# Kernel tuning notes

Measured on AMD Instinct MI355X. Metric: run time of the kernel, lower is better.

Reference implementation:

```python
import jax, jax.numpy as jnp
import numpy as np

EPS = 1e-15


def _trace(t):
    return jnp.einsum('bii->b', t)


def _ortho_loss(ss, k):
    n = jnp.linalg.norm(ss, axis=(-1, -2), keepdims=True)
    diff = ss / n - jnp.eye(k, dtype=ss.dtype) / np.float32(np.sqrt(k))
    return jnp.mean(jnp.linalg.norm(diff, axis=(-1, -2)))


def _mincut_terms(s, adj):
    out_adj = jnp.einsum('bnk,bnm,bml->bkl', s, adj, s)
    d_flat = adj.sum(-1)  # degrees [B,N]
    num = _trace(out_adj)
    den = _trace(jnp.einsum('bnk,bn,bnl->bkl', s, d_flat, s)) + EPS
    return out_adj, num, den, d_flat


def dense_mincut_rewiring(x, adj, s, mask):
    k = s.shape[-1]  # 2
    m = mask[..., None].astype(x.dtype)
    s = jax.nn.softmax(s, axis=-1) * m
    _, num, den, _ = _mincut_terms(s, adj)
    mincut_loss = -jnp.mean(num / den)
    ortho_loss = _ortho_loss(jnp.einsum('bnk,bnl->bkl', s, s), k)
    # laplacian derivative of spectral gap wrt A_uv: (f_u - f_v)^2, f = soft bipartition
    f = s[..., 0]
    dlam = (f[:, :, None] - f[:, None, :]) ** 2
    return adj * (1.0 - dlam), mincut_loss, ortho_loss


def dense_CT_rewiring(x, adj, s, mask):
    k = s.shape[-1]
    m = mask[..., None].astype(x.dtype)
    s = jax.nn.softmax(s, axis=-1) * m
    d_flat = adj.sum(-1)
    sds = _trace(jnp.einsum('bnk,bn,bnl->bkl', s, d_flat, s))
    sas = _trace(jnp.einsum('bnk,bnm,bml->bkl', s, adj, s))
    den = _trace(jnp.einsum('bnk,bnl->bkl', s, s)) + EPS
    ct_loss = jnp.mean((sds - sas) / den)  # tr(Z^T L Z) / tr(Z^T Z)
    ortho_loss = _ortho_loss(jnp.einsum('bnk,bnl->bkl', s, s), k)
    # pairwise CT distances ||z_u - z_v|| / vol(G), sparsified by A
    sq = (s * s).sum(-1)
    d2 = sq[:, :, None] + sq[:, None, :] - 2.0 * jnp.einsum('bnk,bmk->bnm', s, s)
    ct_dist = jnp.sqrt(jnp.maximum(d2, 0.0) + 1e-12)
    vol = d_flat.sum(-1)
    new_adj = (ct_dist / (vol[:, None, None] + EPS)) * adj
    return new_adj, ct_loss, ortho_loss


def dense_mincut_pool(x, adj, s, mask):
    k = s.shape[-1]
    m = mask[..., None].astype(x.dtype)
    s = jax.nn.softmax(s, axis=-1) * m
    x = x * m
    out = jnp.einsum('bnk,bnf->bkf', s, x)
    out_adj, num, den, _ = _mincut_terms(s, adj)
    mincut_loss = -jnp.mean(num / den)
    ortho_loss = _ortho_loss(jnp.einsum('bnk,bnl->bkl', s, s), k)
    out_adj = out_adj * (1.0 - jnp.eye(k, dtype=adj.dtype))  # zero diagonal
    d = jnp.sqrt(out_adj.sum(-1)) + EPS  # [B,k]
    out_adj = out_adj / d[:, None, :] / d[:, :, None]
    return out, out_adj, mincut_loss, ortho_loss


def _dgc(x, adj, w_rel, b_rel, w_root):
    # DenseGraphConv(aggr='add'): lin_rel(A @ x) + lin_root(x)
    return jnp.matmul(adj, x) @ w_rel + b_rel + x @ w_root


def setup_inputs() -> dict:
    B, N, IN, H, KC, OUT, KMC = 16, 1024, 128, 32, 32, 10, 16
    keys = iter(jax.random.split(jax.random.key(0), 48))

    def lin(fin, fout):
        lim = float(1.0 / np.sqrt(fin))
        return (jax.random.uniform(next(keys), (fin, fout), jnp.float32, -lim, lim),
                jax.random.uniform(next(keys), (fout,), jnp.float32, -lim, lim))

    x = jax.random.normal(next(keys), (B, N, IN), jnp.float32)
    u = jax.random.uniform(next(keys), (B, N, N), jnp.float32)
    a = (u < 0.0156).astype(jnp.float32)  # avg degree ~16
    adj = jnp.maximum(a, jnp.swapaxes(a, 1, 2)) * (1.0 - jnp.eye(N, dtype=jnp.float32))
    mask = jnp.ones((B, N), dtype=bool)
    W1, b1 = lin(IN, H)
    Wrw, brw = lin(H, 2)
    Wg_rel, bg = lin(H, H); Wg_root, _ = lin(H, H)
    Wmcg, bmcg = lin(H, KMC)
    W2g_rel, b2g = lin(H, H); W2g_root, _ = lin(H, H)
    Wct, bct = lin(H, KC)
    Wc_rel, bc = lin(H, H); Wc_root, _ = lin(H, H)
    Wmcc, bmcc = lin(H, KMC)
    Wcat, bcat = lin(2 * H, H)
    W2, b2 = lin(H, H)
    W3, b3 = lin(H, OUT)
    return dict(x=x, adj=adj, mask=mask, W1=W1, b1=b1, Wrw=Wrw, brw=brw,
                Wg_rel=Wg_rel, bg=bg, Wg_root=Wg_root, Wmcg=Wmcg, bmcg=bmcg,
                W2g_rel=W2g_rel, b2g=b2g, W2g_root=W2g_root, Wct=Wct, bct=bct,
                Wc_rel=Wc_rel, bc=bc, Wc_root=Wc_root, Wmcc=Wmcc, bmcc=bmcc,
                Wcat=Wcat, bcat=bcat, W2=W2, b2=b2, W3=W3, b3=b3)


def reference(x, adj, mask, W1, b1, Wrw, brw, Wg_rel, bg, Wg_root, Wmcg, bmcg,
              W2g_rel, b2g, W2g_root, Wct, bct, Wc_rel, bc, Wc_root, Wmcc, bmcc,
              Wcat, bcat, W2, b2, W3, b3):
    x = x @ W1 + b1
    # GAP branch
    adj_gap, mc_rw, ol_rw = dense_mincut_rewiring(x, adj, x @ Wrw + brw, mask)
    x_gap = _dgc(x, adj_gap, Wg_rel, bg, Wg_root)
    x_gap, adj_gap, mc1, ol1 = dense_mincut_pool(x_gap, adj_gap, x_gap @ Wmcg + bmcg, mask)
    x_gap = _dgc(x_gap, adj_gap, W2g_rel, b2g, W2g_root)
    # CT branch
    adj_ct, ct_loss, ol_ct = dense_CT_rewiring(x, adj, x @ Wct + bct, mask)
    x_ct = _dgc(x, adj_ct, Wc_rel, bc, Wc_root)
    x_ct, adj_ct, mc2, ol2 = dense_mincut_pool(x_ct, adj_ct, x_ct @ Wmcc + bmcc, mask)
    x_ct = _dgc(x_ct, adj_ct, W2g_rel, b2g, W2g_root)  # source reuses self.conv2gap here
    h = jax.nn.relu(jnp.concatenate([x_gap, x_ct], axis=2) @ Wcat + bcat).sum(axis=1)
    h = jax.nn.relu(h @ W2 + b2)
    logits = h @ W3 + b3
    main_loss = mc_rw + ct_loss + mc1 + mc2
    ortho_loss = ol_rw + ol_ct + ol1 + ol2
    return (jax.nn.log_softmax(logits, axis=-1), main_loss, ortho_loss)
```

## Files before the change

### kernel.cpp

```cpp
#include <hip/hip_runtime.h>
#include <math.h>

#define BB   16
#define NNODE 1024
#define INF_ 128
#define HH   32
#define KMC  16
#define CAP  128
#define EPS15 1e-15f

typedef float v4f __attribute__((ext_vector_type(4)));

#define OFF_X      0
#define OFF_SRW    524288
#define OFF_SQCT   557056
#define OFF_SCT    573440
#define OFF_D      1097728
#define OFF_NUMRW  1114112
#define OFF_SAS    1130496
#define OFF_DGAP   1146880
#define OFF_DCT    1163264
#define OFF_YGAP   1179648
#define OFF_YCT    1703936
#define OFF_XGAP   2228224
#define OFF_XCT    2752512
#define OFF_S2G    3276800
#define OFF_S2C    3538944
#define OFF_TG     3801088
#define OFF_TC     4063232
#define OFF_FROB   4325376
#define OFF_VOL    4325888
#define OFF_MCRW   4325904
#define OFF_CTB    4325920
#define OFF_OLRW   4325936
#define OFF_OLCT   4325952
#define OFF_MC1    4325968
#define OFF_MC2    4325984
#define OFF_OL1    4326000
#define OFF_OL2    4326016
#define OFF_OUTG   4326032
#define OFF_OUTC   4334224
#define OFF_G2G    4342416
#define OFF_G2C    4346512
#define OFF_OAG    4350608
#define OFF_OAC    4354704
#define OFF_ENNZ   4358800
#define OFF_EIDX   4375184
#define OFF_EWG    5423760
#define OFF_EWC    7520912
#define OFF_PACK   9618064

__device__ __forceinline__ float wave_sum(float v) {
#pragma unroll
  for (int off = 32; off >= 1; off >>= 1) v += __shfl_xor(v, off, 64);
  return v;
}

__device__ __forceinline__ float blk_sum(float v, float* sred, int tid) {
  v = wave_sum(v);
  __syncthreads();
  if ((tid & 63) == 0) sred[tid >> 6] = v;
  __syncthreads();
  return sred[0] + sred[1] + sred[2] + sred[3];
}

__global__ __launch_bounds__(256) void k_fused0(
    const float* __restrict__ adj, const float* __restrict__ x,
    const float* __restrict__ W1, const float* __restrict__ b1,
    const float* __restrict__ Wrw, const float* __restrict__ brw,
    const float* __restrict__ Wct, const float* __restrict__ bct,
    float* __restrict__ ws)
{
  __shared__ float sW1[INF_*HH];
  __shared__ float sWct[HH*HH];
  __shared__ float sWrw[HH*2];
  __shared__ float sb1[HH], sbct[HH], sbrw[2];
  __shared__ float sx[8*INF_];
  __shared__ float sX[8*HH];
  __shared__ unsigned int s_e32[4][4][CAP/2];
  int tid = threadIdx.x;
  if (blockIdx.x < 1024) {
    int w = tid >> 6, lane = tid & 63;
    int row0 = blockIdx.x * 16 + w * 4;
    v4f v[16];
#pragma unroll
    for (int rr = 0; rr < 4; rr++) {
      const v4f* ar = (const v4f*)(adj + (size_t)(row0 + rr) * NNODE);
#pragma unroll
      for (int it = 0; it < 4; it++)
        v[rr*4 + it] = __builtin_nontemporal_load(&ar[it*64 + lane]);
    }
#pragma unroll
    for (int rr = 0; rr < 4; rr++) {
      int row = row0 + rr;
      int c = 0;
#pragma unroll
      for (int it = 0; it < 4; it++) {
        v4f a4 = v[rr*4 + it];
        c += (a4.x != 0.f) + (a4.y != 0.f) + (a4.z != 0.f) + (a4.w != 0.f);
      }
      int p = c;
#pragma unroll
      for (int off = 1; off < 64; off <<= 1) {
        int t = __shfl_up(p, off, 64);
        if (lane >= off) p += t;
      }
      int excl = p - c;
      int total = __shfl(p, 63, 64);
      unsigned short* es = (unsigned short*)s_e32[w][rr];
      int pos = excl;
#pragma unroll
      for (int it = 0; it < 4; it++) {
        v4f a4 = v[rr*4 + it];
        int m0 = it*256 + lane*4;
        if (a4.x != 0.f) { if (pos < CAP) es[pos] = (unsigned short)(m0+0); pos++; }
        if (a4.y != 0.f) { if (pos < CAP) es[pos] = (unsigned short)(m0+1); pos++; }
        if (a4.z != 0.f) { if (pos < CAP) es[pos] = (unsigned short)(m0+2); pos++; }
        if (a4.w != 0.f) { if (pos < CAP) es[pos] = (unsigned short)(m0+3); pos++; }
      }
      int nnzc = total < CAP ? total : CAP;
      __syncthreads();
      unsigned int* dst = (unsigned int*)((unsigned short*)(ws + OFF_EIDX) + (size_t)row*CAP);
      int n32 = (nnzc + 1) >> 1;
      if (lane < n32) dst[lane] = s_e32[w][rr][lane];
      if (lane == 0) {
        ((int*)(ws + OFF_ENNZ))[row] = nnzc;
        ws[OFF_D + row] = (float)total;
      }
    }
  } else {
    for (int i = tid; i < INF_*HH; i += 256) sW1[i] = W1[i];
    for (int i = tid; i < HH*HH; i += 256) sWct[i] = Wct[i];
    if (tid < HH*2) sWrw[tid] = Wrw[tid];
    if (tid < HH) { sb1[tid] = b1[tid]; sbct[tid] = bct[tid]; }
    if (tid < 2) sbrw[tid] = brw[tid];
    size_t row0 = (size_t)(blockIdx.x - 1024) * 8;
    ((float4*)sx)[tid] = ((const float4*)(x + row0 * INF_))[tid];
    __syncthreads();
    int r = tid >> 5, h = tid & 31;
    float acc = sb1[h];
#pragma unroll 8
    for (int k = 0; k < INF_; k++) acc += sx[r*INF_ + k] * sW1[k*HH + h];
    size_t row = row0 + r;
    ws[OFF_X + row*HH + h] = acc;
    sX[r*HH + h] = acc;
    __syncthreads();
    float sraw = sbct[h];
#pragma unroll
    for (int k = 0; k < HH; k++) sraw += sX[r*HH + k] * sWct[k*HH + h];
    float mx = sraw;
#pragma unroll
    for (int off = 16; off >= 1; off >>= 1) mx = fmaxf(mx, __shfl_xor(mx, off, 32));
    float e = __expf(sraw - mx);
    float sum = e;
#pragma unroll
    for (int off = 16; off >= 1; off >>= 1) sum += __shfl_xor(sum, off, 32);
    float sv = e / sum;
    ws[OFF_SCT + row*HH + h] = sv;
    float sq = sv * sv;
#pragma unroll
    for (int off = 16; off >= 1; off >>= 1) sq += __shfl_xor(sq, off, 32);
    float xv = sX[r*HH + h];
    float t0 = xv * sWrw[h*2 + 0];
    float t1 = xv * sWrw[h*2 + 1];
#pragma unroll
    for (int off = 16; off >= 1; off >>= 1) { t0 += __shfl_xor(t0, off, 32); t1 += __shfl_xor(t1, off, 32); }
    if (h == 0) {
      ws[OFF_SQCT + row] = sq;
      float r0 = t0 + sbrw[0], r1 = t1 + sbrw[1];
      float m2 = fmaxf(r0, r1);
      float e0 = __expf(r0 - m2), e1 = __expf(r1 - m2);
      float inv = 1.0f / (e0 + e1);
      float s0 = e0*inv, s1 = e1*inv;
      ((float2*)(ws + OFF_SRW))[row] = make_float2(s0, s1);
      ((float4*)(ws + OFF_PACK))[row] = make_float4(s0, s1, sq, 0.f);
    }
  }
}

__global__ __launch_bounds__(256) void k_edge(float* __restrict__ ws)
{
  __shared__ int   s_m[4][CAP];
  __shared__ float s_wg[4][CAP];
  __shared__ float s_wc[4][CAP];
  __shared__ float sp[8][32];
  __shared__ float sred[4];
  int tid = threadIdx.x;
  if (blockIdx.x < 4096) {
    int xcd = blockIdx.x & 7;
    int idx = blockIdx.x >> 3;
    int b = xcd*2 + (idx >> 8);
    int chunk = idx & 255;
    const float* X = ws + OFF_X;
    const float2* srw = (const float2*)(ws + OFF_SRW);
    const float* sqct = ws + OFF_SQCT;
    const float* sct = ws + OFF_SCT;
    const float4* pack = (const float4*)(ws + OFF_PACK) + (size_t)b*NNODE;
    int w = tid >> 6, lane = tid & 63;
    int row = b*NNODE + chunk*4 + w;
    int nnz = ((const int*)(ws + OFF_ENNZ))[row];
    const unsigned short* eidx = (const unsigned short*)(ws + OFF_EIDX) + (size_t)row*CAP;
    const float4* cn4 = (const float4*)(sct + (size_t)row * HH);
    float4 c[8];
#pragma unroll
    for (int i = 0; i < 8; i++) c[i] = cn4[i];
    float2 srwn = srw[row];
    float f_n = srwn.x;
    float sq_n = sqct[row];
    float numrw_p = 0.f, sas_p = 0.f, dg_p = 0.f, dc_p = 0.f;
    for (int e = lane; e < nnz; e += 64) {
      int m = eidx[e];
      s_m[w][e] = m;
      const float4* cm4 = (const float4*)(sct + ((size_t)b*NNODE + m) * HH);
      float dot = 0.f;
#pragma unroll
      for (int i = 0; i < 8; i++) {
        float4 d4 = cm4[i];
        dot += c[i].x*d4.x + c[i].y*d4.y + c[i].z*d4.z + c[i].w*d4.w;
      }
      float4 pk = pack[m];
      numrw_p += srwn.x*pk.x + srwn.y*pk.y;
      float df = f_n - pk.x;
      float wg = 1.0f - df*df;
      float d2 = sq_n + pk.z - 2.0f*dot;
      float wc = sqrtf(fmaxf(d2, 0.0f) + 1e-12f);
      sas_p += dot;
      dg_p += wg;
      dc_p += wc;
      s_wg[w][e] = wg;
      s_wc[w][e] = wc;
      size_t eo = (size_t)row*CAP + e;
      ws[OFF_EWG + eo] = wg;
      ws[OFF_EWC + eo] = wc;
    }
    float numrw = wave_sum(numrw_p);
    float sas = wave_sum(sas_p);
    float dgp = wave_sum(dg_p);
    float dcp = wave_sum(dc_p);
    if (lane == 0) {
      ws[OFF_NUMRW + row] = numrw;
      ws[OFF_SAS + row] = sas;
      ws[OFF_DGAP + row] = dgp;
      ws[OFF_DCT + row] = dcp;
    }
    __syncthreads();
    int eoff = lane >> 4, hp = lane & 15;
    float yg0 = 0.f, yg1 = 0.f, yc0 = 0.f, yc1 = 0.f;
    for (int e = eoff; e < nnz; e += 4) {
      int m = s_m[w][e];
      float wg = s_wg[w][e], wc = s_wc[w][e];
      float2 xv = ((const float2*)(X + ((size_t)b*NNODE + m)*HH))[hp];
      yg0 += wg*xv.x; yg1 += wg*xv.y;
      yc0 += wc*xv.x; yc1 += wc*xv.y;
    }
    yg0 += __shfl_xor(yg0, 16, 64); yg0 += __shfl_xor(yg0, 32, 64);
    yg1 += __shfl_xor(yg1, 16, 64); yg1 += __shfl_xor(yg1, 32, 64);
    yc0 += __shfl_xor(yc0, 16, 64); yc0 += __shfl_xor(yc0, 32, 64);
    yc1 += __shfl_xor(yc1, 16, 64); yc1 += __shfl_xor(yc1, 32, 64);
    if (eoff == 0) {
      ((float2*)(ws + OFF_YGAP + (size_t)row*HH))[hp] = make_float2(yg0, yg1);
      ((float2*)(ws + OFF_YCT  + (size_t)row*HH))[hp] = make_float2(yc0, yc1);
    }
  } else if (blockIdx.x < 4608) {
    int blk = blockIdx.x - 4096;
    int xcd = blk & 7;
    int idx = blk >> 3;
    int b = xcd*2 + (idx >> 5);
    int i = idx & 31;
    const float* sct = ws + OFF_SCT + (size_t)b*NNODE*HH;
    int j = tid & 31, seg = tid >> 5;
    float acc = 0.f;
    for (int n = seg*128; n < seg*128 + 128; n++)
      acc += sct[n*HH + i] * sct[n*HH + j];
    sp[seg][j] = acc;
    __syncthreads();
    if (tid < 32) {
      float g = 0.f;
#pragma unroll
      for (int s = 0; s < 8; s++) g += sp[s][tid];
      float p = g * g;
#pragma unroll
      for (int off = 16; off >= 1; off >>= 1) p += __shfl_xor(p, off, 32);
      if (tid == 0) ws[OFF_FROB + b*32 + i] = p;
    }
  } else {
    int b = blockIdx.x - 4608;
    for (int i = tid; i < 2048; i += 256) ws[OFF_OUTG + b*2048 + i] = 0.f;
    float vp = 0.f;
    for (int n = tid; n < NNODE; n += 256) vp += ws[OFF_D + (size_t)b*NNODE + n];
    float vol = blk_sum(vp, sred, tid);
    if (tid == 0) ws[OFF_VOL + b] = vol;
  }
}

__global__ __launch_bounds__(256) void k_feat(
    const float* __restrict__ Wg_rel, const float* __restrict__ bg, const float* __restrict__ Wg_root,
    const float* __restrict__ Wc_rel, const float* __restrict__ bc, const float* __restrict__ Wc_root,
    const float* __restrict__ Wmcg, const float* __restrict__ bmcg,
    const float* __restrict__ Wmcc, const float* __restrict__ bmcc,
    float* __restrict__ ws)
{
  __shared__ float sWgrel[HH*HH], sWgroot[HH*HH], sWcrel[HH*HH], sWcroot[HH*HH];
  __shared__ float sWmcg[HH*KMC], sWmcc[HH*KMC];
  __shared__ float sbg[HH], sbc[HH], sbmcg[KMC], sbmcc[KMC];
  __shared__ float syg[8*HH], syc[8*HH], sXl[8*HH], sxg[8*HH], sxc[8*HH];
  int tid = threadIdx.x;
  for (int i = tid; i < HH*HH; i += 256) {
    sWgrel[i] = Wg_rel[i]; sWgroot[i] = Wg_root[i];
    sWcrel[i] = Wc_rel[i]; sWcroot[i] = Wc_root[i];
  }
  for (int i = tid; i < HH*KMC; i += 256) { sWmcg[i] = Wmcg[i]; sWmcc[i] = Wmcc[i]; }
  if (tid < HH) { sbg[tid] = bg[tid]; sbc[tid] = bc[tid]; }
  if (tid < KMC) { sbmcg[tid] = bmcg[tid]; sbmcc[tid] = bmcc[tid]; }
  size_t row0 = (size_t)blockIdx.x * 8;
  int b = (int)(row0 >> 10);
  syg[tid] = ws[OFF_YGAP + row0*HH + tid];
  syc[tid] = ws[OFF_YCT + row0*HH + tid];
  sXl[tid] = ws[OFF_X + row0*HH + tid];
  __syncthreads();
  float ivol = 1.0f / (ws[OFF_VOL + b] + EPS15);
  int r = tid >> 5, h = tid & 31;
  float accg = 0.f, accg2 = 0.f, accc = 0.f, accc2 = 0.f;
#pragma unroll
  for (int k = 0; k < HH; k++) {
    float ygv = syg[r*HH + k], Xv = sXl[r*HH + k], ycv = syc[r*HH + k];
    accg  += ygv * sWgrel[k*HH + h];
    accg2 += Xv  * sWgroot[k*HH + h];
    accc  += ycv * sWcrel[k*HH + h];
    accc2 += Xv  * sWcroot[k*HH + h];
  }
  float xgv = sbg[h] + accg + accg2;
  float xcv = sbc[h] + ivol*accc + accc2;
  size_t row = row0 + r;
  ws[OFF_XGAP + row*HH + h] = xgv;
  ws[OFF_XCT + row*HH + h] = xcv;
  sxg[r*HH + h] = xgv;
  sxc[r*HH + h] = xcv;
  __syncthreads();
  int j = h & 15, halfsel = h >> 4;
  const float* sin_ = halfsel ? sxc : sxg;
  const float* sw = halfsel ? sWmcc : sWmcg;
  float raw = halfsel ? sbmcc[j] : sbmcg[j];
#pragma unroll
  for (int k = 0; k < HH; k++) raw += sin_[r*HH + k] * sw[k*KMC + j];
  float mx = raw;
#pragma unroll
  for (int off = 8; off >= 1; off >>= 1) mx = fmaxf(mx, __shfl_xor(mx, off, 16));
  float e = __expf(raw - mx);
  float sum = e;
#pragma unroll
  for (int off = 8; off >= 1; off >>= 1) sum += __shfl_xor(sum, off, 16);
  float sv = e / sum;
  if (halfsel == 0) ws[OFF_S2G + row*KMC + j] = sv;
  else              ws[OFF_S2C + row*KMC + j] = sv;
}

__global__ __launch_bounds__(256) void k_pass2c(float* __restrict__ ws)
{
  int tid = threadIdx.x;
  int xcd = blockIdx.x & 7;
  int idx = blockIdx.x >> 3;
  int b = xcd*2 + (idx >> 8);
  int chunk = idx & 255;
  int row = b*NNODE + chunk*4 + (tid >> 6);
  int lane = tid & 63;
  int nnz = ((const int*)(ws + OFF_ENNZ))[row];
  const unsigned short* eidx = (const unsigned short*)(ws + OFF_EIDX) + (size_t)row*CAP;
  int grp = lane >> 5;
  int el  = lane & 31;
  const float* ew = ws + (grp ? OFF_EWC : OFF_EWG) + (size_t)row*CAP;
  const float* S2 = ws + (grp ? OFF_S2C : OFF_S2G) + (size_t)b*NNODE*KMC;
  float acc[16];
#pragma unroll
  for (int i = 0; i < 16; i++) acc[i] = 0.f;
  for (int e = el; e < nnz; e += 32) {
    int m = eidx[e];
    float wv = ew[e];
    const float4* p = (const float4*)(S2 + m*KMC);
    float4 q0 = p[0], q1 = p[1], q2 = p[2], q3 = p[3];
    acc[0] += wv*q0.x; acc[1] += wv*q0.y; acc[2]  += wv*q0.z; acc[3]  += wv*q0.w;
    acc[4] += wv*q1.x; acc[5] += wv*q1.y; acc[6]  += wv*q1.z; acc[7]  += wv*q1.w;
    acc[8] += wv*q2.x; acc[9] += wv*q2.y; acc[10] += wv*q2.z; acc[11] += wv*q2.w;
    acc[12]+= wv*q3.x; acc[13]+= wv*q3.y; acc[14] += wv*q3.z; acc[15] += wv*q3.w;
  }
#pragma unroll
  for (int off = 1; off < 32; off <<= 1) {
#pragma unroll
    for (int i = 0; i < 16; i++) acc[i] += __shfl_xor(acc[i], off, 32);
  }
  if (el == 0) {
    float* tp = ws + (grp ? OFF_TC : OFF_TG) + (size_t)row*KMC;
#pragma unroll
    for (int i = 0; i < 4; i++)
      ((float4*)tp)[i] = make_float4(acc[4*i], acc[4*i+1], acc[4*i+2], acc[4*i+3]);
  }
}

__global__ __launch_bounds__(256) void k_red2(float* __restrict__ ws)
{
  __shared__ float sg[64*16], sc[64*16], stg[64*16], stc[64*16];
  __shared__ float sxg[64*32], sxc[64*32];
  int b = blockIdx.x >> 4, chunk = blockIdx.x & 15;
  int tid = threadIdx.x;
  size_t n0 = (size_t)b * NNODE + chunk * 64;
  const float* pG  = ws + OFF_S2G  + n0 * KMC;
  const float* pC  = ws + OFF_S2C  + n0 * KMC;
  const float* pTG = ws + OFF_TG   + n0 * KMC;
  const float* pTC = ws + OFF_TC   + n0 * KMC;
  const float* pXG = ws + OFF_XGAP + n0 * HH;
  const float* pXC = ws + OFF_XCT  + n0 * HH;
#pragma unroll
  for (int i = 0; i < 4; i++) {
    sg [tid + i*256] = pG [tid + i*256];
    sc [tid + i*256] = pC [tid + i*256];
    stg[tid + i*256] = pTG[tid + i*256];
    stc[tid + i*256] = pTC[tid + i*256];
  }
#pragma unroll
  for (int i = 0; i < 8; i++) {
    sxg[tid + i*256] = pXG[tid + i*256];
    sxc[tid + i*256] = pXC[tid + i*256];
  }
  __syncthreads();
  int k0 = tid >> 5, h0 = tid & 31;
  float og0 = 0.f, og1 = 0.f, oc0 = 0.f, oc1 = 0.f;
#pragma unroll 8
  for (int r = 0; r < 64; r++) {
    float xgv = sxg[r*32 + h0], xcv = sxc[r*32 + h0];
    og0 += sg[r*16 + k0]     * xgv;
    og1 += sg[r*16 + k0 + 8] * xgv;
    oc0 += sc[r*16 + k0]     * xcv;
    oc1 += sc[r*16 + k0 + 8] * xcv;
  }
  atomicAdd(&ws[OFF_OUTG + b*512 + k0*32 + h0],       og0);
  atomicAdd(&ws[OFF_OUTG + b*512 + (k0+8)*32 + h0],   og1);
  atomicAdd(&ws[OFF_OUTC + b*512 + k0*32 + h0],       oc0);
  atomicAdd(&ws[OFF_OUTC + b*512 + (k0+8)*32 + h0],   oc1);
  int k = tid >> 4, l = tid & 15;
  float gg = 0.f, gc = 0.f, ag = 0.f, ac = 0.f;
#pragma unroll 8
  for (int r = 0; r < 64; r++) {
    float sgk = sg[r*16 + k], sck = sc[r*16 + k];
    gg += sgk * sg [r*16 + l];
    gc += sck * sc [r*16 + l];
    ag += sgk * stg[r*16 + l];
    ac += sck * stc[r*16 + l];
  }
  atomicAdd(&ws[OFF_G2G + b*256 + tid], gg);
  atomicAdd(&ws[OFF_G2C + b*256 + tid], gc);
  atomicAdd(&ws[OFF_OAG + b*256 + tid], ag);
  atomicAdd(&ws[OFF_OAC + b*256 + tid], ac);
}

__global__ __launch_bounds__(256) void k_batch2(
    const float* __restrict__ W2g_rel, const float* __restrict__ b2g, const float* __restrict__ W2g_root,
    const float* __restrict__ Wcat, const float* __restrict__ bcat,
    const float* __restrict__ W2, const float* __restrict__ b2,
    const float* __restrict__ W3, const float* __restrict__ b3,
    float* __restrict__ out, float* __restrict__ ws)
{
  __shared__ float sOAg[256], sOAc[256], sOutg[512], sOutc[512];
  __shared__ float sW2grel[1024], sW2groot[1024], sWcat[2048], sW2l[1024];
  __shared__ float sPg[512], sPc[512], sXg2[512], sXc2[512], sHt[512];
  __shared__ float sHs[32], sH2[32], sLg[16], sScal[2];
  __shared__ float sdkg[16], sdkc[16];
  __shared__ float sred[4];
  int b = blockIdx.x, tid = threadIdx.x;
  sOAg[tid] = ws[OFF_OAG + b*256 + tid];
  sOAc[tid] = ws[OFF_OAC + b*256 + tid];
  sOutg[tid] = ws[OFF_OUTG + b*512 + tid];
  sOutg[tid + 256] = ws[OFF_OUTG + b*512 + tid + 256];
  sOutc[tid] = ws[OFF_OUTC + b*512 + tid];
  sOutc[tid + 256] = ws[OFF_OUTC + b*512 + tid + 256];
  for (int i = tid; i < 1024; i += 256) { sW2grel[i] = W2g_rel[i]; sW2groot[i] = W2g_root[i]; sW2l[i] = W2[i]; }
  for (int i = tid; i < 2048; i += 256) sWcat[i] = Wcat[i];
  size_t base = (size_t)b * NNODE;
  const float2* srw = (const float2*)(ws + OFF_SRW);
  float den1_p = 0, den2_p = 0, trg_p = 0, trc_p = 0;
  float denrw_p=0, num_p=0, sds_p=0, sas_p=0, denct_p=0, g00_p=0, g01_p=0, g11_p=0;
  for (int n = tid; n < NNODE; n += 256) {
    float dg = ws[OFF_DGAP + base + n], dc = ws[OFF_DCT + base + n];
    const float* pg = ws + OFF_S2G + (base + n)*KMC;
    const float* pc = ws + OFF_S2C + (base + n)*KMC;
    float ng = 0.f, nc = 0.f;
#pragma unroll
    for (int j = 0; j < KMC; j++) { ng += pg[j]*pg[j]; nc += pc[j]*pc[j]; }
    den1_p += dg * ng; den2_p += dc * nc; trg_p += ng; trc_p += nc;
    float d = ws[OFF_D + base + n];
    float2 s = srw[base + n];
    float sq = ws[OFF_SQCT + base + n];
    denrw_p += d * (s.x*s.x + s.y*s.y);
    num_p += ws[OFF_NUMRW + base + n];
    sds_p += d * sq;
    sas_p += ws[OFF_SAS + base + n];
    denct_p += sq;
    g00_p += s.x*s.x; g01_p += s.x*s.y; g11_p += s.y*s.y;
  }
  float den1 = blk_sum(den1_p, sred, tid);
  float den2u = blk_sum(den2_p, sred, tid);
  float trg = blk_sum(trg_p, sred, tid);
  float trc = blk_sum(trc_p, sred, tid);
  float denrw = blk_sum(denrw_p, sred, tid);
  float num = blk_sum(num_p, sred, tid);
  float sds = blk_sum(sds_p, sred, tid);
  float sas = blk_sum(sas_p, sred, tid);
  float denct = blk_sum(denct_p, sred, tid);
  float g00 = blk_sum(g00_p, sred, tid);
  float g01 = blk_sum(g01_p, sred, tid);
  float g11 = blk_sum(g11_p, sred, tid);
  float frob_p = (tid < 32) ? ws[OFF_FROB + b*32 + tid] : 0.f;
  float frob2 = blk_sum(frob_p, sred, tid);
  float gv = ws[OFF_G2G + b*256 + tid];
  float cv = ws[OFF_G2C + b*256 + tid];
  float frobg2 = blk_sum(gv*gv, sred, tid);
  float frobc2 = blk_sum(cv*cv, sred, tid);
  float t1_p = (tid < 16) ? sOAg[tid*17] : 0.f;
  float t2_p = (tid < 16) ? sOAc[tid*17] : 0.f;
  float num1 = blk_sum(t1_p, sred, tid);
  float num2u = blk_sum(t2_p, sred, tid);
  float vol = ws[OFF_VOL + b];
  float ivol = 1.0f / (vol + EPS15);
  if (tid == 0) {
    ws[OFF_MCRW + b] = -num / (denrw + EPS15);
    ws[OFF_CTB + b] = (sds - sas) / (denct + EPS15);
    float nrw = sqrtf(g00*g00 + 2.f*g01*g01 + g11*g11);
    ws[OFF_OLRW + b] = sqrtf(fmaxf(2.f - 2.f*(g00 + g11)/(nrw*1.41421356237f), 0.f));
    float nct = sqrtf(frob2);
    ws[OFF_OLCT + b] = sqrtf(fmaxf(2.f - 2.f*denct/(nct*5.65685424949f), 0.f));
    ws[OFF_MC1 + b] = -num1 / (den1 + EPS15);
    ws[OFF_MC2 + b] = -(num2u*ivol) / (den2u*ivol + EPS15);
    ws[OFF_OL1 + b] = sqrtf(fmaxf(2.f - 2.f*trg/(sqrtf(frobg2)*4.f), 0.f));
    ws[OFF_OL2 + b] = sqrtf(fmaxf(2.f - 2.f*trc/(sqrtf(frobc2)*4.f), 0.f));
  }
  sOAc[tid] *= ivol;
  __syncthreads();
  if (tid < 16) { sOAg[tid*17] = 0.f; sOAc[tid*17] = 0.f; }
  __syncthreads();
  if (tid < 16) {
    float rg = 0.f, rc = 0.f;
#pragma unroll
    for (int l = 0; l < 16; l++) { rg += sOAg[tid*16 + l]; rc += sOAc[tid*16 + l]; }
    sdkg[tid] = sqrtf(rg) + EPS15;
    sdkc[tid] = sqrtf(rc) + EPS15;
  }
  __syncthreads();
  { int k = tid >> 4, l = tid & 15;
    sOAg[tid] /= (sdkg[k]*sdkg[l]);
    sOAc[tid] /= (sdkc[k]*sdkc[l]); }
  __syncthreads();
  { int k = tid >> 5, h = tid & 31;
    float p0 = 0, p1 = 0, q0 = 0, q1 = 0;
#pragma unroll
    for (int l = 0; l < 16; l++) {
      p0 += sOAg[k*16 + l] * sOutg[l*32 + h];
      p1 += sOAg[(k+8)*16 + l] * sOutg[l*32 + h];
      q0 += sOAc[k*16 + l] * sOutc[l*32 + h];
      q1 += sOAc[(k+8)*16 + l] * sOutc[l*32 + h];
    }
    sPg[k*32 + h] = p0; sPg[(k+8)*32 + h] = p1;
    sPc[k*32 + h] = q0; sPc[(k+8)*32 + h] = q1;
  }
  __syncthreads();
  { int k = tid >> 5, h = tid & 31;
    float bb2 = b2g[h];
    float a0 = bb2, a1 = bb2, c0 = bb2, c1 = bb2;
#pragma unroll
    for (int q = 0; q < 32; q++) {
      float wr = sW2grel[q*32 + h], wo = sW2groot[q*32 + h];
      a0 += sPg[k*32 + q]*wr + sOutg[k*32 + q]*wo;
      a1 += sPg[(k+8)*32 + q]*wr + sOutg[(k+8)*32 + q]*wo;
      c0 += sPc[k*32 + q]*wr + sOutc[k*32 + q]*wo;
      c1 += sPc[(k+8)*32 + q]*wr + sOutc[(k+8)*32 + q]*wo;
    }
    sXg2[k*32 + h] = a0; sXg2[(k+8)*32 + h] = a1;
    sXc2[k*32 + h] = c0; sXc2[(k+8)*32 + h] = c1;
  }
  __syncthreads();
  { int k = tid >> 5, h = tid & 31;
    float bb = bcat[h];
    float t0 = bb, t1 = bb;
#pragma unroll
    for (int q = 0; q < 32; q++) {
      float w1v = sWcat[q*32 + h], w2v = sWcat[(q+32)*32 + h];
      t0 += sXg2[k*32 + q]*w1v + sXc2[k*32 + q]*w2v;
      t1 += sXg2[(k+8)*32 + q]*w1v + sXc2[(k+8)*32 + q]*w2v;
    }
    sHt[k*32 + h] = fmaxf(t0, 0.f);
    sHt[(k+8)*32 + h] = fmaxf(t1, 0.f);
  }
  __syncthreads();
  if (tid < 32) {
    float s = 0.f;
#pragma unroll
    for (int k = 0; k < 16; k++) s += sHt[k*32 + tid];
    sHs[tid] = s;
  }
  __syncthreads();
  if (tid < 32) {
    float a = b2[tid];
#pragma unroll
    for (int q = 0; q < 32; q++) a += sHs[q]*sW2l[q*32 + tid];
    sH2[tid] = fmaxf(a, 0.f);
  }
  __syncthreads();
  if (tid < 10) {
    float a = b3[tid];
#pragma unroll
    for (int q = 0; q < 32; q++) a += sH2[q]*W3[q*10 + tid];
    sLg[tid] = a;
  }
  __syncthreads();
  if (tid == 0) {
    float m = sLg[0];
    for (int o = 1; o < 10; o++) m = fmaxf(m, sLg[o]);
    float se = 0.f;
    for (int o = 0; o < 10; o++) se += __expf(sLg[o] - m);
    sScal[0] = m; sScal[1] = logf(se);
  }
  __syncthreads();
  if (tid < 10) out[b*10 + tid] = sLg[tid] - sScal[0] - sScal[1];
}

__global__ void k_loss(float* __restrict__ out, const float* __restrict__ ws)
{
  int t = threadIdx.x;
  float vm = 0.f, vo = 0.f;
  if (t < BB) {
    vm = ws[OFF_MCRW + t] + ws[OFF_CTB + t] + ws[OFF_MC1 + t] + ws[OFF_MC2 + t];
    vo = ws[OFF_OLRW + t] + ws[OFF_OLCT + t] + ws[OFF_OL1 + t] + ws[OFF_OL2 + t];
  }
  vm = wave_sum(vm);
  vo = wave_sum(vo);
  if (t == 0) { out[160] = vm / 16.f; out[161] = vo / 16.f; }
}

extern "C" void kernel_launch(void* const* d_in, const int* in_sizes, int n_in,
                              void* d_out, int out_size, void* d_ws, size_t ws_size,
                              hipStream_t stream)
{
  const float* x       = (const float*)d_in[0];
  const float* adj     = (const float*)d_in[1];
  const float* W1      = (const float*)d_in[3];
  const float* b1      = (const float*)d_in[4];
  const float* Wrw     = (const float*)d_in[5];
  const float* brw     = (const float*)d_in[6];
  const float* Wg_rel  = (const float*)d_in[7];
  const float* bg      = (const float*)d_in[8];
  const float* Wg_root = (const float*)d_in[9];
  const float* Wmcg    = (const float*)d_in[10];
  const float* bmcg    = (const float*)d_in[11];
  const float* W2g_rel = (const float*)d_in[12];
  const float* b2g     = (const float*)d_in[13];
  const float* W2g_root= (const float*)d_in[14];
  const float* Wct     = (const float*)d_in[15];
  const float* bct     = (const float*)d_in[16];
  const float* Wc_rel  = (const float*)d_in[17];
  const float* bc      = (const float*)d_in[18];
  const float* Wc_root = (const float*)d_in[19];
  const float* Wmcc    = (const float*)d_in[20];
  const float* bmcc    = (const float*)d_in[21];
  const float* Wcat    = (const float*)d_in[22];
  const float* bcat    = (const float*)d_in[23];
  const float* W2      = (const float*)d_in[24];
  const float* b2      = (const float*)d_in[25];
  const float* W3      = (const float*)d_in[26];
  const float* b3      = (const float*)d_in[27];
  float* out = (float*)d_out;
  float* ws  = (float*)d_ws;

  k_fused0<<<dim3(3072), dim3(256), 0, stream>>>(adj, x, W1, b1, Wrw, brw, Wct, bct, ws);
  k_edge<<<dim3(4624), dim3(256), 0, stream>>>(ws);
  k_feat<<<dim3(2048), dim3(256), 0, stream>>>(Wg_rel, bg, Wg_root, Wc_rel, bc, Wc_root,
                                               Wmcg, bmcg, Wmcc, bmcc, ws);
  k_pass2c<<<dim3(4096), dim3(256), 0, stream>>>(ws);
  k_red2<<<dim3(256), dim3(256), 0, stream>>>(ws);
  k_batch2<<<dim3(16), dim3(256), 0, stream>>>(W2g_rel, b2g, W2g_root, Wcat, bcat,
                                               W2, b2, W3, b3, out, ws);
  k_loss<<<dim3(1), dim3(64), 0, stream>>>(out, ws);
}
```

Measured before the change: 256.4 us.

## Fuse feature transform into edge kernel and merge pass/reduce kernels

Folds the per-node feature transform and second softmax into the edge kernel, so the Y aggregates stay in shared memory and each block computes the batch volume itself. The edge aggregation over S2 is merged with the pooled-reduction kernel into one 512-thread kernel, and the final loss kernel is replaced by atomics inside the batch kernel. The 17 block reductions are batched into a single synchronisation. Together this cuts the launch count from seven to four and removes several global round trips. In exchange every edge block reloads about 18 KB of weights and recomputes the volume sum, and the atomic loss accumulation depends on out[160..161] being zeroed earlier in the edge kernel.

```diff
diff --git a/kernel.cpp b/kernel.cpp
--- a/kernel.cpp
+++ b/kernel.cpp
@@ -64,6 +64,22 @@
   return sred[0] + sred[1] + sred[2] + sred[3];
 }
 
+__device__ __forceinline__ void blk_sum17(float* v, float (*sm)[4], int tid) {
+  int w = tid >> 6, lane = tid & 63;
+#pragma unroll
+  for (int i = 0; i < 17; i++) {
+#pragma unroll
+    for (int off = 32; off >= 1; off >>= 1) v[i] += __shfl_xor(v[i], off, 64);
+  }
+  if (lane == 0) {
+#pragma unroll
+    for (int i = 0; i < 17; i++) sm[i][w] = v[i];
+  }
+  __syncthreads();
+#pragma unroll
+  for (int i = 0; i < 17; i++) v[i] = sm[i][0] + sm[i][1] + sm[i][2] + sm[i][3];
+}
+
 __global__ __launch_bounds__(256) void k_fused0(
     const float* __restrict__ adj, const float* __restrict__ x,
     const float* __restrict__ W1, const float* __restrict__ b1,
@@ -71,11 +87,11 @@
     const float* __restrict__ Wct, const float* __restrict__ bct,
     float* __restrict__ ws)
 {
-  __shared__ float sW1[INF_*HH];
-  __shared__ float sWct[HH*HH];
+  __shared__ __align__(16) float sW1[INF_*HH];
+  __shared__ __align__(16) float sWct[HH*HH];
   __shared__ float sWrw[HH*2];
   __shared__ float sb1[HH], sbct[HH], sbrw[2];
-  __shared__ float sx[8*INF_];
+  __shared__ __align__(16) float sx[8*INF_];
   __shared__ float sX[8*HH];
   __shared__ unsigned int s_e32[4][4][CAP/2];
   int tid = threadIdx.x;
@@ -129,8 +145,9 @@
       }
     }
   } else {
-    for (int i = tid; i < INF_*HH; i += 256) sW1[i] = W1[i];
-    for (int i = tid; i < HH*HH; i += 256) sWct[i] = Wct[i];
+    for (int i = tid; i < INF_*HH/4; i += 256)
+      ((float4*)sW1)[i] = ((const float4*)W1)[i];
+    ((float4*)sWct)[tid] = ((const float4*)Wct)[tid];
     if (tid < HH*2) sWrw[tid] = Wrw[tid];
     if (tid < HH) { sb1[tid] = b1[tid]; sbct[tid] = bct[tid]; }
     if (tid < 2) sbrw[tid] = brw[tid];
@@ -178,26 +195,49 @@
   }
 }
 
-__global__ __launch_bounds__(256) void k_edge(float* __restrict__ ws)
+__global__ __launch_bounds__(256) void k_edgefeat(
+    const float* __restrict__ Wg_rel, const float* __restrict__ bg, const float* __restrict__ Wg_root,
+    const float* __restrict__ Wc_rel, const float* __restrict__ bc, const float* __restrict__ Wc_root,
+    const float* __restrict__ Wmcg, const float* __restrict__ bmcg,
+    const float* __restrict__ Wmcc, const float* __restrict__ bmcc,
+    float* __restrict__ out, float* __restrict__ ws)
 {
   __shared__ int   s_m[4][CAP];
   __shared__ float s_wg[4][CAP];
   __shared__ float s_wc[4][CAP];
   __shared__ float sp[8][32];
   __shared__ float sred[4];
+  __shared__ __align__(16) float sWgrel[HH*HH], sWgroot[HH*HH], sWcrel[HH*HH], sWcroot[HH*HH];
+  __shared__ __align__(16) float sWmcg[HH*KMC], sWmcc[HH*KMC];
+  __shared__ float sbg[HH], sbc[HH], sbmcg[KMC], sbmcc[KMC];
+  __shared__ float sYg[4*HH], sYc[4*HH], sXr[4*HH], sxg[4*HH], sxc[4*HH];
   int tid = threadIdx.x;
   if (blockIdx.x < 4096) {
     int xcd = blockIdx.x & 7;
     int idx = blockIdx.x >> 3;
     int b = xcd*2 + (idx >> 8);
     int chunk = idx & 255;
+    int base4 = b*NNODE + chunk*4;
+    ((float4*)sWgrel)[tid]  = ((const float4*)Wg_rel)[tid];
+    ((float4*)sWgroot)[tid] = ((const float4*)Wg_root)[tid];
+    ((float4*)sWcrel)[tid]  = ((const float4*)Wc_rel)[tid];
+    ((float4*)sWcroot)[tid] = ((const float4*)Wc_root)[tid];
+    if (tid < 128) { ((float4*)sWmcg)[tid] = ((const float4*)Wmcg)[tid];
+                     ((float4*)sWmcc)[tid] = ((const float4*)Wmcc)[tid]; }
+    if (tid < HH)  { sbg[tid] = bg[tid]; sbc[tid] = bc[tid]; }
+    if (tid < KMC) { sbmcg[tid] = bmcg[tid]; sbmcc[tid] = bmcc[tid]; }
+    if (tid < 128) sXr[tid] = ws[OFF_X + (size_t)base4*HH + tid];
+    float vp = 0.f;
+#pragma unroll
+    for (int i = 0; i < 4; i++) vp += ws[OFF_D + (size_t)b*NNODE + tid + i*256];
+
     const float* X = ws + OFF_X;
     const float2* srw = (const float2*)(ws + OFF_SRW);
     const float* sqct = ws + OFF_SQCT;
     const float* sct = ws + OFF_SCT;
     const float4* pack = (const float4*)(ws + OFF_PACK) + (size_t)b*NNODE;
     int w = tid >> 6, lane = tid & 63;
-    int row = b*NNODE + chunk*4 + w;
+    int row = base4 + w;
     int nnz = ((const int*)(ws + OFF_ENNZ))[row];
     const unsigned short* eidx = (const unsigned short*)(ws + OFF_EIDX) + (size_t)row*CAP;
     const float4* cn4 = (const float4*)(sct + (size_t)row * HH);
@@ -258,8 +298,50 @@
     yc0 += __shfl_xor(yc0, 16, 64); yc0 += __shfl_xor(yc0, 32, 64);
     yc1 += __shfl_xor(yc1, 16, 64); yc1 += __shfl_xor(yc1, 32, 64);
     if (eoff == 0) {
-      ((float2*)(ws + OFF_YGAP + (size_t)row*HH))[hp] = make_float2(yg0, yg1);
-      ((float2*)(ws + OFF_YCT  + (size_t)row*HH))[hp] = make_float2(yc0, yc1);
+      sYg[w*HH + 2*hp] = yg0; sYg[w*HH + 2*hp + 1] = yg1;
+      sYc[w*HH + 2*hp] = yc0; sYc[w*HH + 2*hp + 1] = yc1;
+    }
+    float vol = blk_sum(vp, sred, tid);
+    float ivol = 1.0f / (vol + EPS15);
+    if (tid < 128) {
+      int r = tid >> 5, h = tid & 31;
+      float accg = 0.f, accg2 = 0.f, accc = 0.f, accc2 = 0.f;
+#pragma unroll
+      for (int k = 0; k < HH; k++) {
+        float ygv = sYg[r*HH + k], Xv = sXr[r*HH + k], ycv = sYc[r*HH + k];
+        accg  += ygv * sWgrel[k*HH + h];
+        accg2 += Xv  * sWgroot[k*HH + h];
+        accc  += ycv * sWcrel[k*HH + h];
+        accc2 += Xv  * sWcroot[k*HH + h];
+      }
+      float xgv = sbg[h] + accg + accg2;
+      float xcv = sbc[h] + ivol*accc + accc2;
+      size_t rw = (size_t)base4 + r;
+      ws[OFF_XGAP + rw*HH + h] = xgv;
+      ws[OFF_XCT  + rw*HH + h] = xcv;
+      sxg[r*HH + h] = xgv;
+      sxc[r*HH + h] = xcv;
+    }
+    __syncthreads();
+    if (tid < 128) {
+      int r = tid >> 5, h = tid & 31;
+      int j = h & 15, halfsel = h >> 4;
+      const float* sin_ = halfsel ? sxc : sxg;
+      const float* sw = halfsel ? sWmcc : sWmcg;
+      float raw = halfsel ? sbmcc[j] : sbmcg[j];
+#pragma unroll
+      for (int k = 0; k < HH; k++) raw += sin_[r*HH + k] * sw[k*KMC + j];
+      float mx = raw;
+#pragma unroll
+      for (int off = 8; off >= 1; off >>= 1) mx = fmaxf(mx, __shfl_xor(mx, off, 16));
+      float e = __expf(raw - mx);
+      float sum = e;
+#pragma unroll
+      for (int off = 8; off >= 1; off >>= 1) sum += __shfl_xor(sum, off, 16);
+      float sv = e / sum;
+      size_t rw = (size_t)base4 + r;
+      if (halfsel == 0) ws[OFF_S2G + rw*KMC + j] = sv;
+      else              ws[OFF_S2C + rw*KMC + j] = sv;
     }
   } else if (blockIdx.x < 4608) {
     int blk = blockIdx.x - 4096;
@@ -285,6 +367,7 @@
     }
   } else {
     int b = blockIdx.x - 4608;
+    if (b == 0 && tid < 2) out[160 + tid] = 0.f;
     for (int i = tid; i < 2048; i += 256) ws[OFF_OUTG + b*2048 + i] = 0.f;
     float vp = 0.f;
     for (int n = tid; n < NNODE; n += 256) vp += ws[OFF_D + (size_t)b*NNODE + n];
@@ -293,163 +376,79 @@
   }
 }
 
-__global__ __launch_bounds__(256) void k_feat(
-    const float* __restrict__ Wg_rel, const float* __restrict__ bg, const float* __restrict__ Wg_root,
-    const float* __restrict__ Wc_rel, const float* __restrict__ bc, const float* __restrict__ Wc_root,
-    const float* __restrict__ Wmcg, const float* __restrict__ bmcg,
-    const float* __restrict__ Wmcc, const float* __restrict__ bmcc,
-    float* __restrict__ ws)
+__global__ __launch_bounds__(512) void k_passred(float* __restrict__ ws)
 {
-  __shared__ float sWgrel[HH*HH], sWgroot[HH*HH], sWcrel[HH*HH], sWcroot[HH*HH];
-  __shared__ float sWmcg[HH*KMC], sWmcc[HH*KMC];
-  __shared__ float sbg[HH], sbc[HH], sbmcg[KMC], sbmcc[KMC];
-  __shared__ float syg[8*HH], syc[8*HH], sXl[8*HH], sxg[8*HH], sxc[8*HH];
+  __shared__ float sg[32*16], sc[32*16], stg[32*16], stc[32*16];
+  __shared__ float sxg[32*32], sxc[32*32];
+  int b = blockIdx.x >> 5, chunk = blockIdx.x & 31;
   int tid = threadIdx.x;
-  for (int i = tid; i < HH*HH; i += 256) {
-    sWgrel[i] = Wg_rel[i]; sWgroot[i] = Wg_root[i];
-    sWcrel[i] = Wc_rel[i]; sWcroot[i] = Wc_root[i];
-  }
-  for (int i = tid; i < HH*KMC; i += 256) { sWmcg[i] = Wmcg[i]; sWmcc[i] = Wmcc[i]; }
-  if (tid < HH) { sbg[tid] = bg[tid]; sbc[tid] = bc[tid]; }
-  if (tid < KMC) { sbmcg[tid] = bmcg[tid]; sbmcc[tid] = bmcc[tid]; }
-  size_t row0 = (size_t)blockIdx.x * 8;
-  int b = (int)(row0 >> 10);
-  syg[tid] = ws[OFF_YGAP + row0*HH + tid];
-  syc[tid] = ws[OFF_YCT + row0*HH + tid];
-  sXl[tid] = ws[OFF_X + row0*HH + tid];
-  __syncthreads();
-  float ivol = 1.0f / (ws[OFF_VOL + b] + EPS15);
-  int r = tid >> 5, h = tid & 31;
-  float accg = 0.f, accg2 = 0.f, accc = 0.f, accc2 = 0.f;
-#pragma unroll
-  for (int k = 0; k < HH; k++) {
-    float ygv = syg[r*HH + k], Xv = sXl[r*HH + k], ycv = syc[r*HH + k];
-    accg  += ygv * sWgrel[k*HH + h];
-    accg2 += Xv  * sWgroot[k*HH + h];
-    accc  += ycv * sWcrel[k*HH + h];
-    accc2 += Xv  * sWcroot[k*HH + h];
-  }
-  float xgv = sbg[h] + accg + accg2;
-  float xcv = sbc[h] + ivol*accc + accc2;
-  size_t row = row0 + r;
-  ws[OFF_XGAP + row*HH + h] = xgv;
-  ws[OFF_XCT + row*HH + h] = xcv;
-  sxg[r*HH + h] = xgv;
-  sxc[r*HH + h] = xcv;
-  __syncthreads();
-  int j = h & 15, halfsel = h >> 4;
-  const float* sin_ = halfsel ? sxc : sxg;
-  const float* sw = halfsel ? sWmcc : sWmcg;
-  float raw = halfsel ? sbmcc[j] : sbmcg[j];
-#pragma unroll
-  for (int k = 0; k < HH; k++) raw += sin_[r*HH + k] * sw[k*KMC + j];
-  float mx = raw;
-#pragma unroll
-  for (int off = 8; off >= 1; off >>= 1) mx = fmaxf(mx, __shfl_xor(mx, off, 16));
-  float e = __expf(raw - mx);
-  float sum = e;
-#pragma unroll
-  for (int off = 8; off >= 1; off >>= 1) sum += __shfl_xor(sum, off, 16);
-  float sv = e / sum;
-  if (halfsel == 0) ws[OFF_S2G + row*KMC + j] = sv;
-  else              ws[OFF_S2C + row*KMC + j] = sv;
-}
-
-__global__ __launch_bounds__(256) void k_pass2c(float* __restrict__ ws)
-{
-  int tid = threadIdx.x;
-  int xcd = blockIdx.x & 7;
-  int idx = blockIdx.x >> 3;
-  int b = xcd*2 + (idx >> 8);
-  int chunk = idx & 255;
-  int row = b*NNODE + chunk*4 + (tid >> 6);
-  int lane = tid & 63;
-  int nnz = ((const int*)(ws + OFF_ENNZ))[row];
-  const unsigned short* eidx = (const unsigned short*)(ws + OFF_EIDX) + (size_t)row*CAP;
-  int grp = lane >> 5;
-  int el  = lane & 31;
-  const float* ew = ws + (grp ? OFF_EWC : OFF_EWG) + (size_t)row*CAP;
-  const float* S2 = ws + (grp ? OFF_S2C : OFF_S2G) + (size_t)b*NNODE*KMC;
-  float acc[16];
-#pragma unroll
-  for (int i = 0; i < 16; i++) acc[i] = 0.f;
-  for (int e = el; e < nnz; e += 32) {
-    int m = eidx[e];
-    float wv = ew[e];
-    const float4* p = (const float4*)(S2 + m*KMC);
-    float4 q0 = p[0], q1 = p[1], q2 = p[2], q3 = p[3];
-    acc[0] += wv*q0.x; acc[1] += wv*q0.y; acc[2]  += wv*q0.z; acc[3]  += wv*q0.w;
-    acc[4] += wv*q1.x; acc[5] += wv*q1.y; acc[6]  += wv*q1.z; acc[7]  += wv*q1.w;
-    acc[8] += wv*q2.x; acc[9] += wv*q2.y; acc[10] += wv*q2.z; acc[11] += wv*q2.w;
-    acc[12]+= wv*q3.x; acc[13]+= wv*q3.y; acc[14] += wv*q3.z; acc[15] += wv*q3.w;
-  }
-#pragma unroll
-  for (int off = 1; off < 32; off <<= 1) {
-#pragma unroll
-    for (int i = 0; i < 16; i++) acc[i] += __shfl_xor(acc[i], off, 32);
-  }
-  if (el == 0) {
-    float* tp = ws + (grp ? OFF_TC : OFF_TG) + (size_t)row*KMC;
-#pragma unroll
-    for (int i = 0; i < 4; i++)
-      ((float4*)tp)[i] = make_float4(acc[4*i], acc[4*i+1], acc[4*i+2], acc[4*i+3]);
-  }
-}
-
-__global__ __launch_bounds__(256) void k_red2(float* __restrict__ ws)
-{
-  __shared__ float sg[64*16], sc[64*16], stg[64*16], stc[64*16];
-  __shared__ float sxg[64*32], sxc[64*32];
-  int b = blockIdx.x >> 4, chunk = blockIdx.x & 15;
-  int tid = threadIdx.x;
-  size_t n0 = (size_t)b * NNODE + chunk * 64;
+  size_t n0 = (size_t)b * NNODE + chunk * 32;
   const float* pG  = ws + OFF_S2G  + n0 * KMC;
   const float* pC  = ws + OFF_S2C  + n0 * KMC;
-  const float* pTG = ws + OFF_TG   + n0 * KMC;
-  const float* pTC = ws + OFF_TC   + n0 * KMC;
   const float* pXG = ws + OFF_XGAP + n0 * HH;
   const float* pXC = ws + OFF_XCT  + n0 * HH;
+  sg[tid] = pG[tid];
+  sc[tid] = pC[tid];
+  sxg[tid] = pXG[tid]; sxg[tid + 512] = pXG[tid + 512];
+  sxc[tid] = pXC[tid]; sxc[tid + 512] = pXC[tid + 512];
+  int w = tid >> 6, lane = tid & 63;
+  int grp = lane >> 5;
+  int sl  = (lane >> 4) & 1;
+  int k   = lane & 15;
+  const float* S2 = ws + (grp ? OFF_S2C : OFF_S2G) + (size_t)b * NNODE * KMC;
+  float* sT = grp ? stc : stg;
 #pragma unroll
   for (int i = 0; i < 4; i++) {
-    sg [tid + i*256] = pG [tid + i*256];
-    sc [tid + i*256] = pC [tid + i*256];
-    stg[tid + i*256] = pTG[tid + i*256];
-    stc[tid + i*256] = pTC[tid + i*256];
-  }
-#pragma unroll
-  for (int i = 0; i < 8; i++) {
-    sxg[tid + i*256] = pXG[tid + i*256];
-    sxc[tid + i*256] = pXC[tid + i*256];
-  }
-  __syncthreads();
-  int k0 = tid >> 5, h0 = tid & 31;
-  float og0 = 0.f, og1 = 0.f, oc0 = 0.f, oc1 = 0.f;
-#pragma unroll 8
-  for (int r = 0; r < 64; r++) {
-    float xgv = sxg[r*32 + h0], xcv = sxc[r*32 + h0];
-    og0 += sg[r*16 + k0]     * xgv;
-    og1 += sg[r*16 + k0 + 8] * xgv;
-    oc0 += sc[r*16 + k0]     * xcv;
-    oc1 += sc[r*16 + k0 + 8] * xcv;
-  }
-  atomicAdd(&ws[OFF_OUTG + b*512 + k0*32 + h0],       og0);
-  atomicAdd(&ws[OFF_OUTG + b*512 + (k0+8)*32 + h0],   og1);
-  atomicAdd(&ws[OFF_OUTC + b*512 + k0*32 + h0],       oc0);
-  atomicAdd(&ws[OFF_OUTC + b*512 + (k0+8)*32 + h0],   oc1);
-  int k = tid >> 4, l = tid & 15;
-  float gg = 0.f, gc = 0.f, ag = 0.f, ac = 0.f;
-#pragma unroll 8
-  for (int r = 0; r < 64; r++) {
-    float sgk = sg[r*16 + k], sck = sc[r*16 + k];
-    gg += sgk * sg [r*16 + l];
-    gc += sck * sc [r*16 + l];
-    ag += sgk * stg[r*16 + l];
-    ac += sck * stc[r*16 + l];
-  }
-  atomicAdd(&ws[OFF_G2G + b*256 + tid], gg);
-  atomicAdd(&ws[OFF_G2C + b*256 + tid], gc);
-  atomicAdd(&ws[OFF_OAG + b*256 + tid], ag);
-  atomicAdd(&ws[OFF_OAC + b*256 + tid], ac);
+    int rr = w * 4 + i;
+    size_t row = n0 + rr;
+    int nnz = ((const int*)(ws + OFF_ENNZ))[row];
+    const unsigned short* eidx = (const unsigned short*)(ws + OFF_EIDX) + row * CAP;
+    const float* ew = ws + (grp ? OFF_EWC : OFF_EWG) + row * CAP;
+    float acc = 0.f;
+    int e = sl;
+    for (; e + 2 < nnz; e += 4) {
+      int m0 = eidx[e], m1 = eidx[e + 2];
+      float w0 = ew[e], w1 = ew[e + 2];
+      acc += w0 * S2[(size_t)m0 * KMC + k] + w1 * S2[(size_t)m1 * KMC + k];
+    }
+    if (e < nnz) acc += ew[e] * S2[(size_t)eidx[e] * KMC + k];
+    acc += __shfl_xor(acc, 16, 32);
+    if (sl == 0) sT[rr * 16 + k] = acc;
+  }
+  __syncthreads();
+  int sub = tid >> 8, t = tid & 255;
+  { int k0 = t >> 5, h0 = t & 31;
+    float og0 = 0.f, og1 = 0.f, oc0 = 0.f, oc1 = 0.f;
+#pragma unroll
+    for (int i = 0; i < 16; i++) {
+      int r = sub * 16 + i;
+      float xgv = sxg[r*32 + h0], xcv = sxc[r*32 + h0];
+      og0 += sg[r*16 + k0]     * xgv;
+      og1 += sg[r*16 + k0 + 8] * xgv;
+      oc0 += sc[r*16 + k0]     * xcv;
+      oc1 += sc[r*16 + k0 + 8] * xcv;
+    }
+    atomicAdd(&ws[OFF_OUTG + b*512 + k0*32 + h0],     og0);
+    atomicAdd(&ws[OFF_OUTG + b*512 + (k0+8)*32 + h0], og1);
+    atomicAdd(&ws[OFF_OUTC + b*512 + k0*32 + h0],     oc0);
+    atomicAdd(&ws[OFF_OUTC + b*512 + (k0+8)*32 + h0], oc1);
+  }
+  { int kk = t >> 4, l = t & 15;
+    float gg = 0.f, gc = 0.f, ag = 0.f, ac = 0.f;
+#pragma unroll
+    for (int i = 0; i < 16; i++) {
+      int r = sub * 16 + i;
+      float sgk = sg[r*16 + kk], sck = sc[r*16 + kk];
+      gg += sgk * sg [r*16 + l];
+      gc += sck * sc [r*16 + l];
+      ag += sgk * stg[r*16 + l];
+      ac += sck * stc[r*16 + l];
+    }
+    atomicAdd(&ws[OFF_G2G + b*256 + t], gg);
+    atomicAdd(&ws[OFF_G2C + b*256 + t], gc);
+    atomicAdd(&ws[OFF_OAG + b*256 + t], ag);
+    atomicAdd(&ws[OFF_OAC + b*256 + t], ac);
+  }
 }
 
 __global__ __launch_bounds__(256) void k_batch2(
@@ -464,20 +463,21 @@
   __shared__ float sPg[512], sPc[512], sXg2[512], sXc2[512], sHt[512];
   __shared__ float sHs[32], sH2[32], sLg[16], sScal[2];
   __shared__ float sdkg[16], sdkc[16];
-  __shared__ float sred[4];
+  __shared__ float smm[17][4];
   int b = blockIdx.x, tid = threadIdx.x;
   sOAg[tid] = ws[OFF_OAG + b*256 + tid];
   sOAc[tid] = ws[OFF_OAC + b*256 + tid];
-  sOutg[tid] = ws[OFF_OUTG + b*512 + tid];
+  sOutg[tid]       = ws[OFF_OUTG + b*512 + tid];
   sOutg[tid + 256] = ws[OFF_OUTG + b*512 + tid + 256];
-  sOutc[tid] = ws[OFF_OUTC + b*512 + tid];
+  sOutc[tid]       = ws[OFF_OUTC + b*512 + tid];
   sOutc[tid + 256] = ws[OFF_OUTC + b*512 + tid + 256];
   for (int i = tid; i < 1024; i += 256) { sW2grel[i] = W2g_rel[i]; sW2groot[i] = W2g_root[i]; sW2l[i] = W2[i]; }
   for (int i = tid; i < 2048; i += 256) sWcat[i] = Wcat[i];
   size_t base = (size_t)b * NNODE;
   const float2* srw = (const float2*)(ws + OFF_SRW);
-  float den1_p = 0, den2_p = 0, trg_p = 0, trc_p = 0;
-  float denrw_p=0, num_p=0, sds_p=0, sas_p=0, denct_p=0, g00_p=0, g01_p=0, g11_p=0;
+  float v[17];
+#pragma unroll
+  for (int i = 0; i < 17; i++) v[i] = 0.f;
   for (int n = tid; n < NNODE; n += 256) {
     float dg = ws[OFF_DGAP + base + n], dc = ws[OFF_DCT + base + n];
     const float* pg = ws + OFF_S2G + (base + n)*KMC;
@@ -485,52 +485,43 @@
     float ng = 0.f, nc = 0.f;
 #pragma unroll
     for (int j = 0; j < KMC; j++) { ng += pg[j]*pg[j]; nc += pc[j]*pc[j]; }
-    den1_p += dg * ng; den2_p += dc * nc; trg_p += ng; trc_p += nc;
+    v[0] += dg * ng; v[1] += dc * nc; v[2] += ng; v[3] += nc;
     float d = ws[OFF_D + base + n];
     float2 s = srw[base + n];
     float sq = ws[OFF_SQCT + base + n];
-    denrw_p += d * (s.x*s.x + s.y*s.y);
-    num_p += ws[OFF_NUMRW + base + n];
-    sds_p += d * sq;
-    sas_p += ws[OFF_SAS + base + n];
-    denct_p += sq;
-    g00_p += s.x*s.x; g01_p += s.x*s.y; g11_p += s.y*s.y;
-  }
-  float den1 = blk_sum(den1_p, sred, tid);
-  float den2u = blk_sum(den2_p, sred, tid);
-  float trg = blk_sum(trg_p, sred, tid);
-  float trc = blk_sum(trc_p, sred, tid);
-  float denrw = blk_sum(denrw_p, sred, tid);
-  float num = blk_sum(num_p, sred, tid);
-  float sds = blk_sum(sds_p, sred, tid);
-  float sas = blk_sum(sas_p, sred, tid);
-  float denct = blk_sum(denct_p, sred, tid);
-  float g00 = blk_sum(g00_p, sred, tid);
-  float g01 = blk_sum(g01_p, sred, tid);
-  float g11 = blk_sum(g11_p, sred, tid);
-  float frob_p = (tid < 32) ? ws[OFF_FROB + b*32 + tid] : 0.f;
-  float frob2 = blk_sum(frob_p, sred, tid);
+    v[4] += d * (s.x*s.x + s.y*s.y);
+    v[5] += ws[OFF_NUMRW + base + n];
+    v[6] += d * sq;
+    v[7] += ws[OFF_SAS + base + n];
+    v[8] += sq;
+    v[9] += s.x*s.x; v[10] += s.x*s.y; v[11] += s.y*s.y;
+  }
+  v[12] = (tid < 32) ? ws[OFF_FROB + b*32 + tid] : 0.f;
   float gv = ws[OFF_G2G + b*256 + tid];
   float cv = ws[OFF_G2C + b*256 + tid];
-  float frobg2 = blk_sum(gv*gv, sred, tid);
-  float frobc2 = blk_sum(cv*cv, sred, tid);
-  float t1_p = (tid < 16) ? sOAg[tid*17] : 0.f;
-  float t2_p = (tid < 16) ? sOAc[tid*17] : 0.f;
-  float num1 = blk_sum(t1_p, sred, tid);
-  float num2u = blk_sum(t2_p, sred, tid);
+  v[13] = gv*gv; v[14] = cv*cv;
+  __syncthreads();
+  v[15] = (tid < 16) ? sOAg[tid*17] : 0.f;
+  v[16] = (tid < 16) ? sOAc[tid*17] : 0.f;
+  blk_sum17(v, smm, tid);
+  float den1 = v[0], den2u = v[1], trg = v[2], trc = v[3], denrw = v[4], num = v[5],
+        sds = v[6], sas = v[7], denct = v[8], g00 = v[9], g01 = v[10], g11 = v[11],
+        frob2 = v[12], frobg2 = v[13], frobc2 = v[14], num1 = v[15], num2u = v[16];
   float vol = ws[OFF_VOL + b];
   float ivol = 1.0f / (vol + EPS15);
   if (tid == 0) {
-    ws[OFF_MCRW + b] = -num / (denrw + EPS15);
-    ws[OFF_CTB + b] = (sds - sas) / (denct + EPS15);
+    float mcrw = -num / (denrw + EPS15);
+    float ctb  = (sds - sas) / (denct + EPS15);
     float nrw = sqrtf(g00*g00 + 2.f*g01*g01 + g11*g11);
-    ws[OFF_OLRW + b] = sqrtf(fmaxf(2.f - 2.f*(g00 + g11)/(nrw*1.41421356237f), 0.f));
+    float olrw = sqrtf(fmaxf(2.f - 2.f*(g00 + g11)/(nrw*1.41421356237f), 0.f));
     float nct = sqrtf(frob2);
-    ws[OFF_OLCT + b] = sqrtf(fmaxf(2.f - 2.f*denct/(nct*5.65685424949f), 0.f));
-    ws[OFF_MC1 + b] = -num1 / (den1 + EPS15);
-    ws[OFF_MC2 + b] = -(num2u*ivol) / (den2u*ivol + EPS15);
-    ws[OFF_OL1 + b] = sqrtf(fmaxf(2.f - 2.f*trg/(sqrtf(frobg2)*4.f), 0.f));
-    ws[OFF_OL2 + b] = sqrtf(fmaxf(2.f - 2.f*trc/(sqrtf(frobc2)*4.f), 0.f));
+    float olct = sqrtf(fmaxf(2.f - 2.f*denct/(nct*5.65685424949f), 0.f));
+    float mc1 = -num1 / (den1 + EPS15);
+    float mc2 = -(num2u*ivol) / (den2u*ivol + EPS15);
+    float ol1 = sqrtf(fmaxf(2.f - 2.f*trg/(sqrtf(frobg2)*4.f), 0.f));
+    float ol2 = sqrtf(fmaxf(2.f - 2.f*trc/(sqrtf(frobc2)*4.f), 0.f));
+    atomicAdd(out + 160, (mcrw + ctb + mc1 + mc2) * 0.0625f);
+    atomicAdd(out + 161, (olrw + olct + ol1 + ol2) * 0.0625f);
   }
   sOAc[tid] *= ivol;
   __syncthreads();
@@ -619,19 +610,6 @@
   }
   __syncthreads();
   if (tid < 10) out[b*10 + tid] = sLg[tid] - sScal[0] - sScal[1];
-}
-
-__global__ void k_loss(float* __restrict__ out, const float* __restrict__ ws)
-{
-  int t = threadIdx.x;
-  float vm = 0.f, vo = 0.f;
-  if (t < BB) {
-    vm = ws[OFF_MCRW + t] + ws[OFF_CTB + t] + ws[OFF_MC1 + t] + ws[OFF_MC2 + t];
-    vo = ws[OFF_OLRW + t] + ws[OFF_OLCT + t] + ws[OFF_OL1 + t] + ws[OFF_OL2 + t];
-  }
-  vm = wave_sum(vm);
-  vo = wave_sum(vo);
-  if (t == 0) { out[160] = vm / 16.f; out[161] = vo / 16.f; }
 }
 
 extern "C" void kernel_launch(void* const* d_in, const int* in_sizes, int n_in,
@@ -669,12 +647,9 @@
   float* ws  = (float*)d_ws;
 
   k_fused0<<<dim3(3072), dim3(256), 0, stream>>>(adj, x, W1, b1, Wrw, brw, Wct, bct, ws);
-  k_edge<<<dim3(4624), dim3(256), 0, stream>>>(ws);
-  k_feat<<<dim3(2048), dim3(256), 0, stream>>>(Wg_rel, bg, Wg_root, Wc_rel, bc, Wc_root,
-                                               Wmcg, bmcg, Wmcc, bmcc, ws);
-  k_pass2c<<<dim3(4096), dim3(256), 0, stream>>>(ws);
-  k_red2<<<dim3(256), dim3(256), 0, stream>>>(ws);
+  k_edgefeat<<<dim3(4624), dim3(256), 0, stream>>>(Wg_rel, bg, Wg_root, Wc_rel, bc, Wc_root,
+                                                   Wmcg, bmcg, Wmcc, bmcc, out, ws);
+  k_passred<<<dim3(512), dim3(512), 0, stream>>>(ws);
   k_batch2<<<dim3(16), dim3(256), 0, stream>>>(W2g_rel, b2g, W2g_root, Wcat, bcat,
                                                W2, b2, W3, b3, out, ws);
-  k_loss<<<dim3(1), dim3(64), 0, stream>>>(out, ws);
-}
+}
```

Result: no change. 253.2 us (-1.2%).
